# Kernel optimization log

Hardware: AMD Instinct MI355X
Metric: run time of the kernel (lower is better)

Reference implementation:

```python
import jax, jax.numpy as jnp
import numpy as np
from jax import lax

_SIGMAS = [0.5, 1.0, 2.0, 4.0, 8.0]
_FS = int(4 * _SIGMAS[-1] + 1)   # 33
_PAD = int(2 * _SIGMAS[-1])      # 16
_C1 = (0.01 * 1.0) ** 2
_C2 = (0.03 * 1.0) ** 2
_ALPHA = 0.025
_COMP = 200.0
_DR = 1.0


def _gauss2d(size, sigma):
    coords = np.arange(size, dtype=np.float32) - size // 2
    g = np.exp(-coords ** 2 / (2.0 * sigma ** 2))
    g /= g.sum()
    return np.outer(g, g).astype(np.float32)


def _build_g_masks():
    g = np.zeros((3 * len(_SIGMAS), 1, _FS, _FS), dtype=np.float32)
    for i, s in enumerate(_SIGMAS):
        k = _gauss2d(_FS, s)
        for j in range(3):
            g[3 * i + j, 0] = k
    return jnp.asarray(g)


def setup_inputs() -> dict:
    key = jax.random.key(0)
    kx, ky = jax.random.split(key)
    B, C, H, W = 8, 3, 512, 512
    x = jax.random.uniform(kx, (B, C, H, W), dtype=jnp.float32)
    y = jax.random.uniform(ky, (B, C, H, W), dtype=jnp.float32)
    return {"x": x, "y": y, "g_masks": _build_g_masks()}


def _gconv(img, w):
    # grouped conv, 3 groups (one per RGB channel), 'same' padding of 16
    return lax.conv_general_dilated(
        img, w, window_strides=(1, 1), padding=[(_PAD, _PAD), (_PAD, _PAD)],
        dimension_numbers=("NCHW", "OIHW", "NCHW"), feature_group_count=3)


def reference(x, y, g_masks):
    mux = _gconv(x, g_masks)            # [B,15,H,W]
    muy = _gconv(y, g_masks)
    mux2 = mux * mux
    muy2 = muy * muy
    muxy = mux * muy
    sigmax2 = _gconv(x * x, g_masks) - mux2
    sigmay2 = _gconv(y * y, g_masks) - muy2
    sigmaxy = _gconv(x * y, g_masks) - muxy

    l = (2.0 * muxy + _C1) / (mux2 + muy2 + _C1)
    cs = (2.0 * sigmaxy + _C2) / (sigmax2 + sigmay2 + _C2)

    lM = l[:, -1] * l[:, -2] * l[:, -3]   # largest-sigma luminance terms
    PIcs = jnp.prod(cs, axis=1)
    loss_ms_ssim = 1.0 - lM * PIcs        # [B,H,W]

    loss_l1 = jnp.abs(x - y)              # [B,3,H,W]
    gaussian_l1 = _gconv(loss_l1, g_masks[-3:]).mean(axis=1)  # [B,H,W]

    loss_mix = _ALPHA * loss_ms_ssim + (1.0 - _ALPHA) * gaussian_l1 / _DR
    return (_COMP * loss_mix).mean()
```

## Files before the change

### kernel.cpp

```cpp
#include <hip/hip_runtime.h>

typedef _Float16 h2_t __attribute__((ext_vector_type(2)));
typedef _Float16 f16x8 __attribute__((ext_vector_type(8)));
typedef float f32x4 __attribute__((ext_vector_type(4)));
typedef unsigned u32x4 __attribute__((ext_vector_type(4)));

#define DI __device__ __forceinline__

#if __has_builtin(__builtin_amdgcn_sched_barrier)
#define SCHED_FENCE() __builtin_amdgcn_sched_barrier(0)
#else
#define SCHED_FENCE()
#endif

constexpr int PAW = 96;
constexpr int PBV = 72;
constexpr int TILE = 64 * PAW;
constexpr int PLANE = 64 * PBV;
constexpr float kC1 = 1.0e-4f;
constexpr float kC2 = 9.0e-4f;
constexpr float kALPHA = 0.025f;

DI float rcp_fast(float v) { return __builtin_amdgcn_rcpf(v); }

DI float fdot2f(h2_t a, h2_t b, float c) {
#if __has_builtin(__builtin_amdgcn_fdot2)
  return __builtin_amdgcn_fdot2(a, b, c, false);
#else
  return c + (float)(a.x) * (float)(b.x) + (float)(a.y) * (float)(b.y);
#endif
}

DI h2_t w2h(unsigned u) { return __builtin_bit_cast(h2_t, u); }

DI f16x8 ldfrag(const _Float16* __restrict__ p) {
  return *reinterpret_cast<const f16x8*>(p);
}

DI f32x4 mfma16(f16x8 a, f16x8 b, f32x4 c) {
  return __builtin_amdgcn_mfma_f32_16x16x32_f16(a, b, c, 0, 0, 0);
}

DI f16x8 pkabs8(f16x8 v) {
  u32x4 u = __builtin_bit_cast(u32x4, v);
  u32x4 msk = {0x7FFF7FFFu, 0x7FFF7FFFu, 0x7FFF7FFFu, 0x7FFF7FFFu};
  u &= msk;
  return __builtin_bit_cast(f16x8, u);
}

template<bool L1P>
DI void hconv_all(const _Float16* __restrict__ xt, _Float16* __restrict__ hb,
                  f16x8 wA0, f16x8 wA1, int w, int lane) {
  const int q = lane >> 4, m = lane & 15;
  const int K0b = (w < 2) ? 0 : 32;
  const int cb = w * 16 + q * 4;
  f32x4 zero4 = {0.f, 0.f, 0.f, 0.f};
#pragma unroll
  for (int nt = 0; nt < 4; ++nt) {
    const int row = nt * 16 + m;
    const int base = row * PAW + K0b + q * 8;
    f32x4 ax = zero4, ay = zero4, asq = zero4, axy = zero4, al1 = zero4;
#pragma unroll
    for (int ks = 0; ks < 2; ++ks) {
      const f16x8 A = ks ? wA1 : wA0;
      const int idx = (base + ks * 32) ^ ((row & 7) << 3);
      f16x8 xv = ldfrag(xt + idx);
      f16x8 yv = ldfrag(xt + TILE + idx);
      ax = mfma16(A, xv, ax);
      ay = mfma16(A, yv, ay);
      asq = mfma16(A, xv * xv + yv * yv, asq);
      axy = mfma16(A, xv * yv, axy);
      if (L1P) al1 = mfma16(A, pkabs8(xv - yv), al1);
    }
    _Float16* wp = hb + cb * PBV + nt * 16 + m;
#pragma unroll
    for (int j = 0; j < 4; ++j) {
      wp[j * PBV] = (_Float16)ax[j];
      wp[PLANE + j * PBV] = (_Float16)ay[j];
      wp[2 * PLANE + j * PBV] = (_Float16)asq[j];
      wp[3 * PLANE + j * PBV] = (_Float16)axy[j];
      if (L1P) wp[4 * PLANE + j * PBV] = (_Float16)al1[j];
    }
    SCHED_FENCE();
  }
}

DI void vconv_all(const _Float16* __restrict__ hb,
                  f16x8 w00, f16x8 w01, f16x8 w10, f16x8 w11,
                  int w, int lane, f32x4* __restrict__ acc) {
  const int q = lane >> 4, m = lane & 15;
  const int base = (w * 16 + m) * PBV + q * 8;
#pragma unroll
  for (int ks = 0; ks < 2; ++ks) {
    f16x8 B0 = ks ? w01 : w00;
    f16x8 B1 = ks ? w11 : w10;
#pragma unroll
    for (int pl = 0; pl < 4; ++pl) {
      f16x8 A = ldfrag(hb + pl * PLANE + base + ks * 32);
      acc[2 * pl]     = mfma16(A, B0, acc[2 * pl]);
      acc[2 * pl + 1] = mfma16(A, B1, acc[2 * pl + 1]);
    }
    SCHED_FENCE();
  }
}

DI float vl1(const _Float16* __restrict__ hb, const unsigned* __restrict__ U,
             int col, int r0) {
  const _Float16* p0 = hb + 4 * PLANE + col * PBV + r0;
  float s = 0.f;
#pragma unroll
  for (int p = 0; p < 20; ++p)
    s = fdot2f(w2h(U[p]), *reinterpret_cast<const h2_t*>(p0 + 2 * p), s);
  return s;
}

template<bool LAST>
DI void do_sigma_m(int s, const _Float16* __restrict__ frh,
                   const unsigned* __restrict__ U,
                   const _Float16* __restrict__ xt, _Float16* __restrict__ hb,
                   float* __restrict__ PIcs, float& gl1s, int tid) {
  const int lane = tid & 63, w = tid >> 6;
  const f16x8* fr = reinterpret_cast<const f16x8*>(frh) + s * 256 + lane;
  f16x8 w00 = fr[0], w01 = fr[64], w10 = fr[128], w11 = fr[192];
  const bool odd = (w & 1);
  f16x8 wA0 = odd ? w10 : w00;
  f16x8 wA1 = odd ? w11 : w01;

  hconv_all<LAST>(xt, hb, wA0, wA1, w, lane);
  __syncthreads();
  f32x4 zero4 = {0.f, 0.f, 0.f, 0.f};
  f32x4 acc[8];
#pragma unroll
  for (int i = 0; i < 8; ++i) acc[i] = zero4;
  vconv_all(hb, w00, w01, w10, w11, w, lane, acc);
  if (LAST) gl1s += vl1(hb, U, tid & 63, (tid >> 6) * 8);
#pragma unroll
  for (int h = 0; h < 2; ++h)
#pragma unroll
    for (int j = 0; j < 4; ++j) {
      const int i = h * 4 + j;
      float a = acc[h][j], b = acc[2 + h][j];
      float m2 = a * a + b * b, mxy = a * b;
      PIcs[i] *= fmaf(2.f, acc[6 + h][j] - mxy, kC2) *
                 rcp_fast(acc[4 + h][j] - m2 + kC2);
      if (LAST)
        PIcs[i] *= fmaf(2.f, mxy, kC1) * rcp_fast(m2 + kC1);
    }
  __syncthreads();
}

DI unsigned packh(float a, float b) {
  h2_t v; v.x = (_Float16)a; v.y = (_Float16)b;
  return __builtin_bit_cast(unsigned, v);
}

__global__ void prep_k(const float* __restrict__ gm, float* __restrict__ ws) {
  int t = threadIdx.x;
  if (t < 165) {
    int s = t / 33, j = t % 33;
    const float* mk = gm + (3 * s) * (33 * 33);
    ws[t] = mk[16 * 33 + j] / sqrtf(mk[16 * 33 + 16]);
  }
  __syncthreads();
  if (t == 0) {
    const float* w = ws + 4 * 33;
    unsigned* U = (unsigned*)(ws + 168);
    for (int p = 0; p < 20; ++p) {
      float ux = 0.f, uy = 0.f;
      for (int i = 0; i < 4; ++i) {
        int j = p - i;
        if (j < 0 || j > 16) continue;
        ux += w[2 * j];
        if (2 * j + 1 <= 32) uy += w[2 * j + 1];
        if (j > 0) ux += w[2 * j - 1];
        uy += w[2 * j];
      }
      U[p] = packh(ux, uy);
    }
  }
  _Float16* fr = (_Float16*)(ws + 208);
  const int Rs[5] = {4, 6, 12, 16, 16};
  for (int e = t; e < 10240; e += 256) {
    int s = e >> 11, r = e & 2047;
    int cls = (r >> 10) & 1, ks = (r >> 9) & 1, lane = (r >> 3) & 63, i = r & 7;
    int tp = 32 * ks - 16 * cls + 8 * (lane >> 4) + i - (lane & 15);
    int R = Rs[s], j = tp - 16 + R;
    float v = (j >= 0 && j <= 2 * R) ? ws[s * 33 + j] : 0.f;
    fr[e] = (_Float16)v;
  }
}

__global__ __launch_bounds__(256, 2)
void msloss_k(const float* __restrict__ x, const float* __restrict__ y,
              const float* __restrict__ ws, float* __restrict__ out) {
  __shared__ __align__(16) _Float16 smem[2 * TILE + 5 * PLANE];
  __shared__ float red[4];
  _Float16* xt = smem;
  _Float16* hb = smem + 2 * TILE;
  const _Float16* frh = (const _Float16*)(ws + 208);
  const unsigned* U = (const unsigned*)(ws + 168);
  const int tid = threadIdx.x;
  const int ox = blockIdx.x * 64, oy = blockIdx.y * 32;
  const int b = blockIdx.z;

  float PIcs[8];
  float gl1s = 0.f;
#pragma unroll
  for (int i = 0; i < 8; ++i) PIcs[i] = 1.f;

  for (int c = 0; c < 3; ++c) {
    const float* xp = x + (size_t)(b * 3 + c) * (512 * 512);
    const float* yp = y + (size_t)(b * 3 + c) * (512 * 512);
#pragma unroll
    for (int it = 0; it < 12; ++it) {
      int idx = it * 256 + tid;
      int row = idx / 48, cp = idx % 48;
      int gy = oy + row - 16, gx = ox + cp * 2 - 16;
      bool ok = ((unsigned)gy < 512u) && ((unsigned)gx < 512u);
      float2 xv = make_float2(0.f, 0.f), yv = make_float2(0.f, 0.f);
      if (ok) {
        xv = *reinterpret_cast<const float2*>(xp + gy * 512 + gx);
        yv = *reinterpret_cast<const float2*>(yp + gy * 512 + gx);
      }
      h2_t hx; hx.x = (_Float16)xv.x; hx.y = (_Float16)xv.y;
      h2_t hy; hy.x = (_Float16)yv.x; hy.y = (_Float16)yv.y;
      int si = (row * PAW + cp * 2) ^ ((row & 7) << 3);
      *reinterpret_cast<h2_t*>(xt + si) = hx;
      *reinterpret_cast<h2_t*>(xt + TILE + si) = hy;
    }
    __syncthreads();
    do_sigma_m<false>(0, frh, U, xt, hb, PIcs, gl1s, tid);
    do_sigma_m<false>(1, frh, U, xt, hb, PIcs, gl1s, tid);
    do_sigma_m<false>(2, frh, U, xt, hb, PIcs, gl1s, tid);
    do_sigma_m<false>(3, frh, U, xt, hb, PIcs, gl1s, tid);
    do_sigma_m<true >(4, frh, U, xt, hb, PIcs, gl1s, tid);
  }

  float s = ((1.f - kALPHA) / 3.f) * gl1s;
#pragma unroll
  for (int i = 0; i < 8; ++i) s += kALPHA * (1.f - PIcs[i]);
#pragma unroll
  for (int off = 32; off > 0; off >>= 1) s += __shfl_down(s, off);
  if ((tid & 63) == 0) red[tid >> 6] = s;
  __syncthreads();
  if (tid == 0)
    atomicAdd(out, (red[0] + red[1] + red[2] + red[3]) *
                       (200.0f / (8.0f * 512.0f * 512.0f)));
}

extern "C" void kernel_launch(void* const* d_in, const int* in_sizes, int n_in,
                              void* d_out, int out_size, void* d_ws, size_t ws_size,
                              hipStream_t stream) {
  const float* x = (const float*)d_in[0];
  const float* y = (const float*)d_in[1];
  const float* gm = (const float*)d_in[2];
  float* out = (float*)d_out;
  float* ws = (float*)d_ws;

  hipMemsetAsync(d_out, 0, out_size * sizeof(float), stream);
  prep_k<<<1, 256, 0, stream>>>(gm, ws);
  msloss_k<<<dim3(8, 16, 8), 256, 0, stream>>>(x, y, ws, out);
}
```

Measured before the change: 275.8 us.

## Split separable conv into two smem passes to cut LDS and raise occupancy

The horizontal/vertical Gaussian passes now run in two phases. The first phase handles x, y and x²+y² in three planes. The second reuses the same buffer for xy and the L1 term. This cuts the intermediate shared buffer from five planes to three, and launch bounds rise from 2 to 3 blocks per CU for better latency hiding. In exchange there are two extra barriers per sigma, the input tile is read twice, and fewer registers are available per thread.

```diff
diff --git a/kernel.cpp b/kernel.cpp
--- a/kernel.cpp
+++ b/kernel.cpp
@@ -48,9 +48,8 @@
   return __builtin_bit_cast(f16x8, u);
 }
 
-template<bool L1P>
-DI void hconv_all(const _Float16* __restrict__ xt, _Float16* __restrict__ hb,
-                  f16x8 wA0, f16x8 wA1, int w, int lane) {
+DI void hconv_p1(const _Float16* __restrict__ xt, _Float16* __restrict__ hb,
+                 f16x8 wA0, f16x8 wA1, int w, int lane) {
   const int q = lane >> 4, m = lane & 15;
   const int K0b = (w < 2) ? 0 : 32;
   const int cb = w * 16 + q * 4;
@@ -59,7 +58,7 @@
   for (int nt = 0; nt < 4; ++nt) {
     const int row = nt * 16 + m;
     const int base = row * PAW + K0b + q * 8;
-    f32x4 ax = zero4, ay = zero4, asq = zero4, axy = zero4, al1 = zero4;
+    f32x4 ax = zero4, ay = zero4, asq = zero4;
 #pragma unroll
     for (int ks = 0; ks < 2; ++ks) {
       const f16x8 A = ks ? wA1 : wA0;
@@ -69,8 +68,6 @@
       ax = mfma16(A, xv, ax);
       ay = mfma16(A, yv, ay);
       asq = mfma16(A, xv * xv + yv * yv, asq);
-      axy = mfma16(A, xv * yv, axy);
-      if (L1P) al1 = mfma16(A, pkabs8(xv - yv), al1);
     }
     _Float16* wp = hb + cb * PBV + nt * 16 + m;
 #pragma unroll
@@ -78,16 +75,46 @@
       wp[j * PBV] = (_Float16)ax[j];
       wp[PLANE + j * PBV] = (_Float16)ay[j];
       wp[2 * PLANE + j * PBV] = (_Float16)asq[j];
-      wp[3 * PLANE + j * PBV] = (_Float16)axy[j];
-      if (L1P) wp[4 * PLANE + j * PBV] = (_Float16)al1[j];
     }
     SCHED_FENCE();
   }
 }
 
-DI void vconv_all(const _Float16* __restrict__ hb,
-                  f16x8 w00, f16x8 w01, f16x8 w10, f16x8 w11,
-                  int w, int lane, f32x4* __restrict__ acc) {
+template<bool L1P>
+DI void hconv_p2(const _Float16* __restrict__ xt, _Float16* __restrict__ hb,
+                 f16x8 wA0, f16x8 wA1, int w, int lane) {
+  const int q = lane >> 4, m = lane & 15;
+  const int K0b = (w < 2) ? 0 : 32;
+  const int cb = w * 16 + q * 4;
+  f32x4 zero4 = {0.f, 0.f, 0.f, 0.f};
+#pragma unroll
+  for (int nt = 0; nt < 4; ++nt) {
+    const int row = nt * 16 + m;
+    const int base = row * PAW + K0b + q * 8;
+    f32x4 axy = zero4, al1 = zero4;
+#pragma unroll
+    for (int ks = 0; ks < 2; ++ks) {
+      const f16x8 A = ks ? wA1 : wA0;
+      const int idx = (base + ks * 32) ^ ((row & 7) << 3);
+      f16x8 xv = ldfrag(xt + idx);
+      f16x8 yv = ldfrag(xt + TILE + idx);
+      axy = mfma16(A, xv * yv, axy);
+      if (L1P) al1 = mfma16(A, pkabs8(xv - yv), al1);
+    }
+    _Float16* wp = hb + cb * PBV + nt * 16 + m;
+#pragma unroll
+    for (int j = 0; j < 4; ++j) {
+      wp[j * PBV] = (_Float16)axy[j];
+      if (L1P) wp[PLANE + j * PBV] = (_Float16)al1[j];
+    }
+    SCHED_FENCE();
+  }
+}
+
+template<int NPL>
+DI void vconvN(const _Float16* __restrict__ hb,
+               f16x8 w00, f16x8 w01, f16x8 w10, f16x8 w11,
+               int w, int lane, f32x4* __restrict__ acc) {
   const int q = lane >> 4, m = lane & 15;
   const int base = (w * 16 + m) * PBV + q * 8;
 #pragma unroll
@@ -95,7 +122,7 @@
     f16x8 B0 = ks ? w01 : w00;
     f16x8 B1 = ks ? w11 : w10;
 #pragma unroll
-    for (int pl = 0; pl < 4; ++pl) {
+    for (int pl = 0; pl < NPL; ++pl) {
       f16x8 A = ldfrag(hb + pl * PLANE + base + ks * 32);
       acc[2 * pl]     = mfma16(A, B0, acc[2 * pl]);
       acc[2 * pl + 1] = mfma16(A, B1, acc[2 * pl + 1]);
@@ -106,7 +133,7 @@
 
 DI float vl1(const _Float16* __restrict__ hb, const unsigned* __restrict__ U,
              int col, int r0) {
-  const _Float16* p0 = hb + 4 * PLANE + col * PBV + r0;
+  const _Float16* p0 = hb + PLANE + col * PBV + r0;
   float s = 0.f;
 #pragma unroll
   for (int p = 0; p < 20; ++p)
@@ -126,23 +153,30 @@
   f16x8 wA0 = odd ? w10 : w00;
   f16x8 wA1 = odd ? w11 : w01;
 
-  hconv_all<LAST>(xt, hb, wA0, wA1, w, lane);
-  __syncthreads();
   f32x4 zero4 = {0.f, 0.f, 0.f, 0.f};
-  f32x4 acc[8];
-#pragma unroll
-  for (int i = 0; i < 8; ++i) acc[i] = zero4;
-  vconv_all(hb, w00, w01, w10, w11, w, lane, acc);
-  if (LAST) gl1s += vl1(hb, U, tid & 63, (tid >> 6) * 8);
+
+  hconv_p1(xt, hb, wA0, wA1, w, lane);
+  __syncthreads();
+  f32x4 a1[6];
+#pragma unroll
+  for (int i = 0; i < 6; ++i) a1[i] = zero4;
+  vconvN<3>(hb, w00, w01, w10, w11, w, lane, a1);
+  __syncthreads();
+  hconv_p2<LAST>(xt, hb, wA0, wA1, w, lane);
+  __syncthreads();
+  f32x4 a2[2];
+  a2[0] = zero4; a2[1] = zero4;
+  vconvN<1>(hb, w00, w01, w10, w11, w, lane, a2);
+  if (LAST) gl1s += vl1(hb, U, lane, w * 8);
 #pragma unroll
   for (int h = 0; h < 2; ++h)
 #pragma unroll
     for (int j = 0; j < 4; ++j) {
       const int i = h * 4 + j;
-      float a = acc[h][j], b = acc[2 + h][j];
+      float a = a1[h][j], b = a1[2 + h][j];
       float m2 = a * a + b * b, mxy = a * b;
-      PIcs[i] *= fmaf(2.f, acc[6 + h][j] - mxy, kC2) *
-                 rcp_fast(acc[4 + h][j] - m2 + kC2);
+      PIcs[i] *= fmaf(2.f, a2[h][j] - mxy, kC2) *
+                 rcp_fast(a1[4 + h][j] - m2 + kC2);
       if (LAST)
         PIcs[i] *= fmaf(2.f, mxy, kC1) * rcp_fast(m2 + kC1);
     }
@@ -190,10 +224,10 @@
   }
 }
 
-__global__ __launch_bounds__(256, 2)
+__global__ __launch_bounds__(256, 3)
 void msloss_k(const float* __restrict__ x, const float* __restrict__ y,
               const float* __restrict__ ws, float* __restrict__ out) {
-  __shared__ __align__(16) _Float16 smem[2 * TILE + 5 * PLANE];
+  __shared__ __align__(16) _Float16 smem[2 * TILE + 3 * PLANE];
   __shared__ float red[4];
   _Float16* xt = smem;
   _Float16* hb = smem + 2 * TILE;
```

Result: slower. 403.0 us (+46.1%).
